# Kernel tuning notes

Hardware: AMD Instinct MI355X
Metric: run time of the kernel (lower is better)

The kernel has to match this reference:

```python
import jax, jax.numpy as jnp
import numpy as np

TOPK = 64  # init kwarg: number of dst routes kept per src node


def setup_inputs() -> dict:
    key = jax.random.key(0)
    ks = jax.random.split(key, 6)
    B, J, K, D, Dd = 4, 4096, 8192, 64, 64  # batch, src_nodes, dst_nodes, src_dim, dst_dim
    val = jax.random.normal(ks[0], (B, J, D), jnp.float32)
    state = jax.random.normal(ks[1], (B, J), jnp.float32)
    dst_state = jax.random.normal(ks[2], (B, K), jnp.float32)
    dst_val = jax.random.normal(ks[3], (B, K, Dd), jnp.float32)
    W_route = jax.random.normal(ks[4], (D, K), jnp.float32) / np.sqrt(D).astype(np.float32)
    W_val = jax.random.normal(ks[5], (D, Dd), jnp.float32) / np.sqrt(D).astype(np.float32)
    return dict(val=val, state=state, dst_state=dst_state, dst_val=dst_val,
                W_route=W_route, W_val=W_val)


def _sparse_routes(logits, topk):
    # top-k indices per src node, scatter a bool mask, masked softmax over dst axis
    _, idx = jax.lax.top_k(logits, topk)              # [B, J, topk]
    B, J, K = logits.shape
    mask = jnp.zeros((B, J, K), dtype=bool)
    mask = mask.at[jnp.arange(B)[:, None, None],
                   jnp.arange(J)[None, :, None], idx].set(True)
    neg = jnp.finfo(logits.dtype).min
    return jax.nn.softmax(jnp.where(mask, logits, neg), axis=-1)


def reference(val, state, dst_state, dst_val, W_route, W_val):
    # route_fn: linear over src val -> logits [B, J, K]
    logits = jnp.einsum('bjd,dk->bjk', val, W_route)
    routes = _sparse_routes(logits, TOPK)             # sparse masked softmax
    projected_val = jnp.einsum('bjd,de->bje', val, W_val)  # val_proj_fn (Linear)
    projected_state = state                            # state_proj_fn = Identity
    sender = jax.nn.softplus(state)                    # state_activation_fn
    weighted = routes * sender[..., None]              # [B, J, K]
    delta_state = jnp.einsum('bjk,bj->bk', weighted, projected_state)
    delta_val = jnp.einsum('bjk,bjd->bkd', weighted, projected_val)
    # merge_mode='add'
    return (dst_state + delta_state, dst_val + delta_val)
```

## Files before the change

kernel.cpp:

```cpp
#include <hip/hip_runtime.h>
#include <math.h>

#define NB 4
#define J 4096
#define KDIM 8192
#define DDIM 64
#define DD 64
#define TOPK 64

#define BM 32
#define THREADS 512
#define THREADS_SEL 256
#define NITER_H 8
#define CAP_H 128
#define GCAP 256
#define BCAP 96
#define OVFCAP 262144

typedef _Float16 half8_t __attribute__((ext_vector_type(8)));
typedef float f32x16 __attribute__((ext_vector_type(16)));
union H8 { half8_t h; uint4 u; };
__device__ __forceinline__ half8_t as_h8(uint4 v) { H8 x; x.u = v; return x.h; }

__device__ __forceinline__ unsigned f2key(float f) {
  unsigned u = __float_as_uint(f);
  return u ^ (unsigned)(((int)u >> 31) | 0x80000000);
}
__device__ __forceinline__ float key2f(unsigned k) {
  unsigned u = (k & 0x80000000u) ? (k & 0x7FFFFFFFu) : ~k;
  return __uint_as_float(u);
}
__device__ __forceinline__ unsigned wred_maxu(unsigned v) {
  #pragma unroll
  for (int o = 32; o > 0; o >>= 1) { unsigned u = __shfl_xor(v, o, 64); v = u > v ? u : v; }
  return v;
}
__device__ __forceinline__ unsigned wred_minu(unsigned v) {
  #pragma unroll
  for (int o = 32; o > 0; o >>= 1) { unsigned u = __shfl_xor(v, o, 64); v = u < v ? u : v; }
  return v;
}
__device__ __forceinline__ float wred_addf(float v) {
  #pragma unroll
  for (int o = 32; o > 0; o >>= 1) v += __shfl_xor(v, o, 64);
  return v;
}

__device__ __forceinline__ void route_append(
    unsigned* counts, uint2* bucket, unsigned* ovf_cnt, uint2* ovf,
    int b, unsigned kk, unsigned jloc, float w)
{
  const size_t bk = (size_t)b * KDIM + kk;
  const unsigned slot = atomicAdd(&counts[bk], 1u);
  if (slot < BCAP) {
    bucket[bk * BCAP + slot] = make_uint2(__float_as_uint(w), jloc);
  } else {
    const unsigned op = atomicAdd(ovf_cnt, 1u);
    if (op < (unsigned)OVFCAP)
      ovf[op] = make_uint2(__float_as_uint(w), ((unsigned)bk << 12) | jloc);
  }
}

__global__ void k_prep(const float* __restrict__ W, unsigned* __restrict__ WFh,
                       float* __restrict__ WT)
{
  __shared__ _Float16 lh[64][64];
  __shared__ float lf[64][64];
  const int t = threadIdx.x;
  const int kb = blockIdx.x * 64;
  for (int i = t; i < 4096; i += 256) {
    const int d = i >> 6, c = i & 63;
    const float x = W[(size_t)d * KDIM + kb + c];
    lh[c][d] = (_Float16)x;
    lf[c][d] = x;
  }
  __syncthreads();
  for (int q = t; q < 512; q += 256) {
    const int gt2 = q >> 8, rem = q & 255;
    const int ks = rem >> 6, lane = rem & 63;
    const int c = gt2 * 32 + (lane & 31);
    const int d0 = ks * 16 + (lane >> 5) * 8;
    const int gtile = blockIdx.x * 2 + gt2;
    const size_t off = ((size_t)(gtile * 4 + ks) * 64 + lane) * 4;
    *(uint4*)(WFh + off) = *(const uint4*)&lh[c][d0];
  }
  for (int q = t; q < 1024; q += 256) {
    const int c = q >> 4, d0 = (q & 15) * 4;
    *(float4*)(WT + (size_t)(kb + c) * DDIM + d0) = *(const float4*)&lf[c][d0];
  }
}

__global__ __launch_bounds__(THREADS, 4) void k_cand(
    const float* __restrict__ val, const unsigned* __restrict__ WFh,
    const float* __restrict__ W_val, float* __restrict__ pv,
    unsigned short* __restrict__ gidx, unsigned* __restrict__ gcnt,
    float* __restrict__ gtau, unsigned* __restrict__ flags)
{
  __shared__ __align__(16) float val_lds[BM][DDIM + 4];
  __shared__ unsigned short cand_idx[BM][CAP_H];
  __shared__ unsigned have[BM];
  __shared__ float tauF[BM];

  const int t = threadIdx.x;
  const int lane = t & 63;
  const int wv = t >> 6;
  const int hi = lane >> 5;
  const int lane31 = lane & 31;
  const int row0 = blockIdx.x * BM;
  const int h = blockIdx.y;

  {
    const int r = t >> 4, d0 = (t & 15) * 4;
    const float4 v4 = *(const float4*)(val + (size_t)(row0 + r) * DDIM + d0);
    val_lds[r][d0] = v4.x; val_lds[r][d0 + 1] = v4.y;
    val_lds[r][d0 + 2] = v4.z; val_lds[r][d0 + 3] = v4.w;
  }
  __syncthreads();

  if (t < BM) {
    float n2 = 0.f;
    #pragma unroll
    for (int d = 0; d < DDIM; ++d) { const float x = val_lds[t][d]; n2 = fmaf(x, x, n2); }
    tauF[t] = 0.26f * sqrtf(n2);
    have[t] = 0u;
    if (h == 0) gtau[row0 + t] = tauF[t];
  }

  half8_t ah[4];
  {
    const int m = lane31;
    #pragma unroll
    for (int ks = 0; ks < 4; ++ks) {
      const int d0 = ks * 16 + hi * 8;
      #pragma unroll
      for (int j = 0; j < 8; ++j) ah[ks][j] = (_Float16)val_lds[m][d0 + j];
    }
  }
  __syncthreads();

  float taufr[16];
  #pragma unroll
  for (int r = 0; r < 16; ++r) taufr[r] = tauF[(r & 3) + 8 * (r >> 2) + 4 * hi];

  const unsigned* wpBase = WFh + (size_t)(h * 128 + wv * 2) * 1024 + lane * 4;
  const unsigned* wp = wpBase;
  uint4 b0 = *(const uint4*)(wp);        uint4 b1 = *(const uint4*)(wp + 256);
  uint4 b2 = *(const uint4*)(wp + 512);  uint4 b3 = *(const uint4*)(wp + 768);
  uint4 b4 = *(const uint4*)(wp + 1024); uint4 b5 = *(const uint4*)(wp + 1280);
  uint4 b6 = *(const uint4*)(wp + 1536); uint4 b7 = *(const uint4*)(wp + 1792);

  #pragma unroll 1
  for (int it = 0; it < NITER_H; ++it) {
    f32x16 acc0, acc1;
    #pragma unroll
    for (int i = 0; i < 16; ++i) { acc0[i] = 0.f; acc1[i] = 0.f; }
    acc0 = __builtin_amdgcn_mfma_f32_32x32x16_f16(ah[0], as_h8(b0), acc0, 0, 0, 0);
    acc1 = __builtin_amdgcn_mfma_f32_32x32x16_f16(ah[0], as_h8(b4), acc1, 0, 0, 0);
    acc0 = __builtin_amdgcn_mfma_f32_32x32x16_f16(ah[1], as_h8(b1), acc0, 0, 0, 0);
    acc1 = __builtin_amdgcn_mfma_f32_32x32x16_f16(ah[1], as_h8(b5), acc1, 0, 0, 0);
    acc0 = __builtin_amdgcn_mfma_f32_32x32x16_f16(ah[2], as_h8(b2), acc0, 0, 0, 0);
    acc1 = __builtin_amdgcn_mfma_f32_32x32x16_f16(ah[2], as_h8(b6), acc1, 0, 0, 0);
    acc0 = __builtin_amdgcn_mfma_f32_32x32x16_f16(ah[3], as_h8(b3), acc0, 0, 0, 0);
    acc1 = __builtin_amdgcn_mfma_f32_32x32x16_f16(ah[3], as_h8(b7), acc1, 0, 0, 0);

    const unsigned colbase = (unsigned)((h * 128 + it * 16 + wv * 2) * 32 + lane31);

    wp = (it == NITER_H - 1) ? wpBase : wp + 16384;
    b0 = *(const uint4*)(wp);        b1 = *(const uint4*)(wp + 256);
    b2 = *(const uint4*)(wp + 512);  b3 = *(const uint4*)(wp + 768);
    b4 = *(const uint4*)(wp + 1024); b5 = *(const uint4*)(wp + 1280);
    b6 = *(const uint4*)(wp + 1536); b7 = *(const uint4*)(wp + 1792);

    #pragma unroll
    for (int r = 0; r < 16; ++r) {
      const int row = (r & 3) + 8 * (r >> 2) + 4 * hi;
      const float tf = taufr[r];
      if (acc0[r] > tf) {
        const unsigned slot = atomicAdd(&have[row], 1u);
        if (slot < CAP_H) cand_idx[row][slot] = (unsigned short)colbase;
      }
      if (acc1[r] > tf) {
        const unsigned slot = atomicAdd(&have[row], 1u);
        if (slot < CAP_H) cand_idx[row][slot] = (unsigned short)(colbase + 32);
      }
    }
  }

  if (h == 1) {
    const int r = t >> 4, e0 = (t & 15) * 4;
    float a0 = 0.f, a1 = 0.f, a2 = 0.f, a3 = 0.f;
    #pragma unroll 8
    for (int d = 0; d < DDIM; ++d) {
      const float v = val_lds[r][d];
      const float4 w4 = *(const float4*)(W_val + (size_t)d * DD + e0);
      a0 = fmaf(v, w4.x, a0); a1 = fmaf(v, w4.y, a1);
      a2 = fmaf(v, w4.z, a2); a3 = fmaf(v, w4.w, a3);
    }
    *(float4*)(pv + (size_t)(row0 + r) * DD + e0) = make_float4(a0, a1, a2, a3);
  }

  __syncthreads();

  for (int i = t; i < BM * CAP_H; i += THREADS) {
    const int r = i >> 7, s = i & (CAP_H - 1);
    const unsigned hv = have[r];
    const int lim = hv < CAP_H ? (int)hv : CAP_H;
    if (s < lim)
      gidx[(size_t)(row0 + r) * GCAP + h * CAP_H + s] = cand_idx[r][s];
  }
  if (t < BM) {
    const unsigned hv = have[t];
    gcnt[(size_t)(row0 + t) * 2 + h] = hv < CAP_H ? hv : CAP_H;
    if (hv > CAP_H) flags[row0 + t] = 1u;
  }
}

__global__ __launch_bounds__(THREADS_SEL, 4) void k_select(
    const float* __restrict__ val, const float* __restrict__ state,
    const float* __restrict__ WT,
    const unsigned short* __restrict__ gidx, const unsigned* __restrict__ gcnt,
    const float* __restrict__ gtau, unsigned* __restrict__ flags,
    unsigned* __restrict__ counts, uint2* __restrict__ bucket,
    unsigned* __restrict__ ovf_cnt, uint2* __restrict__ ovf)
{
  __shared__ float skey[THREADS_SEL / 64][GCAP];
  const int t = threadIdx.x;
  const int lane = t & 63;
  const int wv = t >> 6;
  const int row = blockIdx.x * (THREADS_SEL / 64) + wv;

  if (flags[row]) return;
  const int c0 = (int)gcnt[(size_t)row * 2];
  const int c1 = (int)gcnt[(size_t)row * 2 + 1];
  const int nc = c0 + c1;
  if (nc < TOPK) { if (lane == 0) flags[row] = 1u; return; }
  const float tau = gtau[row];

  const int cq = lane >> 2;
  const int dq = lane & 3;
  float4 v4[4];
  #pragma unroll
  for (int j = 0; j < 4; ++j)
    v4[j] = *(const float4*)(val + (size_t)row * DDIM + j * 16 + dq * 4);

  const unsigned short* grow = gidx + (size_t)row * GCAP;

  unsigned id4[4];
  #pragma unroll
  for (int i = 0; i < 4; ++i) {
    const int s = i * 64 + lane;
    id4[i] = 0xFFFFFFFFu;
    if (s < nc) {
      const int ps = s < c0 ? s : (s - c0 + CAP_H);
      id4[i] = (unsigned)grow[ps];
    }
  }

  for (int s0 = 0; s0 < nc; s0 += 32) {
    const int sA = s0 + cq;
    const int sB = s0 + 16 + cq;
    const bool okA = sA < nc, okB = sB < nc;
    int psA = sA < c0 ? sA : (sA - c0 + CAP_H); if (!okA) psA = 0;
    int psB = sB < c0 ? sB : (sB - c0 + CAP_H); if (!okB) psB = 0;
    const unsigned kkA = (unsigned)grow[psA] & (KDIM - 1);
    const unsigned kkB = (unsigned)grow[psB] & (KDIM - 1);
    const float* wtA = WT + (size_t)kkA * DDIM + dq * 4;
    const float* wtB = WT + (size_t)kkB * DDIM + dq * 4;
    float4 wA[4], wB[4];
    #pragma unroll
    for (int j = 0; j < 4; ++j) wA[j] = *(const float4*)(wtA + j * 16);
    #pragma unroll
    for (int j = 0; j < 4; ++j) wB[j] = *(const float4*)(wtB + j * 16);
    float aA = 0.f, aB = 0.f;
    #pragma unroll
    for (int j = 0; j < 4; ++j) {
      aA = fmaf(v4[j].x, wA[j].x, aA); aA = fmaf(v4[j].y, wA[j].y, aA);
      aA = fmaf(v4[j].z, wA[j].z, aA); aA = fmaf(v4[j].w, wA[j].w, aA);
      aB = fmaf(v4[j].x, wB[j].x, aB); aB = fmaf(v4[j].y, wB[j].y, aB);
      aB = fmaf(v4[j].z, wB[j].z, aB); aB = fmaf(v4[j].w, wB[j].w, aB);
    }
    aA += __shfl_xor(aA, 1, 64); aA += __shfl_xor(aA, 2, 64);
    aB += __shfl_xor(aB, 1, 64); aB += __shfl_xor(aB, 2, 64);
    if (dq == 0) {
      if (okA) skey[wv][sA] = aA;
      if (okB) skey[wv][sB] = aB;
    }
  }
  asm volatile("s_waitcnt lgkmcnt(0)" ::: "memory");
  __builtin_amdgcn_sched_barrier(0);

  unsigned k4[4];
  #pragma unroll
  for (int i = 0; i < 4; ++i) {
    const int s = i * 64 + lane;
    k4[i] = (s < nc) ? f2key(skey[wv][s]) : 0u;
  }
  unsigned lmax = k4[0];
  #pragma unroll
  for (int i = 1; i < 4; ++i) lmax = k4[i] > lmax ? k4[i] : lmax;
  const unsigned kmaxAll = wred_maxu(lmax);
  unsigned klo = f2key(0.99f * tau); if (klo == 0u) klo = 1u;
  unsigned khi = kmaxAll + 1u;
  auto cge4 = [&](unsigned th) {
    int c = 0;
    #pragma unroll
    for (int i = 0; i < 4; ++i) c += __popcll(__ballot(k4[i] >= th));
    return c;
  };
  int cnt = nc;
  while (cnt != TOPK && khi - klo > 1u) {
    const unsigned mid = klo + ((khi - klo) >> 1);
    const int c = cge4(mid);
    if (c >= TOPK) { klo = mid; cnt = c; } else khi = mid;
  }
  const unsigned thr = klo;
  if (key2f(thr) <= 1.006f * tau) {
    if (lane == 0) flags[row] = 1u;
    return;
  }
  unsigned selmask = 0u;
  if (cnt == TOPK) {
    #pragma unroll
    for (int i = 0; i < 4; ++i) if (k4[i] >= thr) selmask |= 1u << i;
  } else {
    #pragma unroll
    for (int i = 0; i < 4; ++i) if (k4[i] > thr) selmask |= 1u << i;
    int tot = 0;
    #pragma unroll
    for (int i = 0; i < 4; ++i) tot += __popcll(__ballot((selmask >> i) & 1));
    int need = TOPK - tot;
    while (need > 0) {
      unsigned best = 0xFFFFFFFFu; int bi = -1;
      #pragma unroll
      for (int i = 0; i < 4; ++i)
        if (k4[i] == thr && !(selmask & (1u << i)) && id4[i] < best) { best = id4[i]; bi = i; }
      const unsigned g = wred_minu(best);
      if (g == 0xFFFFFFFFu) break;
      if (bi >= 0 && best == g) selmask |= 1u << bi;
      --need;
    }
  }
  const float m = key2f(kmaxAll);
  float p[4]; float lsum = 0.f;
  #pragma unroll
  for (int i = 0; i < 4; ++i) {
    p[i] = 0.f;
    if (selmask & (1u << i)) { p[i] = __expf(key2f(k4[i]) - m); lsum += p[i]; }
  }
  lsum = wred_addf(lsum);
  const float st = state[row];
  const float sender = st > 20.f ? st : log1pf(__expf(st));
  const float scale = sender / lsum;
  const int b = row / J;
  const unsigned jloc = (unsigned)(row & (J - 1));
  #pragma unroll
  for (int i = 0; i < 4; ++i) {
    if (selmask & (1u << i))
      route_append(counts, bucket, ovf_cnt, ovf, b, id4[i], jloc, p[i] * scale);
  }
}

__global__ void k_fix(const float* __restrict__ val, const float* __restrict__ state,
                      const float* __restrict__ W, const unsigned* __restrict__ flags,
                      unsigned* __restrict__ counts, uint2* __restrict__ bucket,
                      unsigned* __restrict__ ovf_cnt, uint2* __restrict__ ovf)
{
  __shared__ unsigned anyf;
  __shared__ unsigned lsk[64][TOPK + 1];
  __shared__ unsigned short lsi[64][TOPK];
  const int t = threadIdx.x;
  const int row = blockIdx.x * 64 + t;
  if (t == 0) anyf = 0u;
  __syncthreads();
  const unsigned f = flags[row];
  if (f) anyf = 1u;
  __syncthreads();
  if (!anyf) return;
  if (!f) return;

  float v[DDIM];
  #pragma unroll
  for (int d = 0; d < DDIM; ++d) v[d] = val[(size_t)row * DDIM + d];
  int m = 0, worst = 0;
  for (int k = 0; k < KDIM; ++k) {
    float acc = 0.f;
    #pragma unroll 8
    for (int d = 0; d < DDIM; ++d) acc = fmaf(v[d], W[(size_t)d * KDIM + k], acc);
    const unsigned key = f2key(acc);
    if (m < TOPK) {
      lsk[t][m] = key; lsi[t][m] = (unsigned short)k; ++m;
      if (m == TOPK) {
        worst = 0;
        for (int q = 1; q < TOPK; ++q)
          if (lsk[t][q] < lsk[t][worst] ||
              (lsk[t][q] == lsk[t][worst] && lsi[t][q] > lsi[t][worst])) worst = q;
      }
    } else if (key > lsk[t][worst]) {
      lsk[t][worst] = key; lsi[t][worst] = (unsigned short)k;
      worst = 0;
      for (int q = 1; q < TOPK; ++q)
        if (lsk[t][q] < lsk[t][worst] ||
            (lsk[t][q] == lsk[t][worst] && lsi[t][q] > lsi[t][worst])) worst = q;
    }
  }
  unsigned km = lsk[t][0];
  for (int q = 1; q < TOPK; ++q) if (lsk[t][q] > km) km = lsk[t][q];
  const float mx = key2f(km);
  float lsum = 0.f;
  for (int q = 0; q < TOPK; ++q) lsum += __expf(key2f(lsk[t][q]) - mx);
  const float st = state[row];
  const float sender = st > 20.f ? st : log1pf(__expf(st));
  const float scale = sender / lsum;
  const int b = row / J;
  const unsigned jloc = (unsigned)(row & (J - 1));
  for (int q = 0; q < TOPK; ++q) {
    const float w = __expf(key2f(lsk[t][q]) - mx) * scale;
    route_append(counts, bucket, ovf_cnt, ovf, b, (unsigned)lsi[t][q], jloc, w);
  }
}

__global__ void k_gather(const unsigned* __restrict__ counts,
                         const uint2* __restrict__ bucket, const float* __restrict__ pv,
                         const float* __restrict__ state,
                         const float* __restrict__ dst_state,
                         const float* __restrict__ dst_val,
                         float* __restrict__ out_state, float* __restrict__ out_val)
{
  const int wv = threadIdx.x >> 6, lane = threadIdx.x & 63;
  const size_t bk = (size_t)blockIdx.x * 4 + wv;
  unsigned n = counts[bk];
  if (n > BCAP) n = BCAP;
  const int b = (int)(bk >> 13);
  const size_t jbase = (size_t)b * J;
  const uint2* __restrict__ bb = bucket + bk * BCAP;
  float a0 = 0.f, a1 = 0.f, a2 = 0.f, a3 = 0.f;
  float s0 = 0.f, s1 = 0.f, s2 = 0.f, s3 = 0.f;
  unsigned i = 0;
  for (; i + 4 <= n; i += 4) {
    const uint2 e0 = bb[i + 0], e1 = bb[i + 1], e2 = bb[i + 2], e3 = bb[i + 3];
    const float w0 = __uint_as_float(e0.x), w1 = __uint_as_float(e1.x);
    const float w2 = __uint_as_float(e2.x), w3 = __uint_as_float(e3.x);
    a0 = fmaf(w0, pv[(jbase + e0.y) * DD + lane], a0);
    a1 = fmaf(w1, pv[(jbase + e1.y) * DD + lane], a1);
    a2 = fmaf(w2, pv[(jbase + e2.y) * DD + lane], a2);
    a3 = fmaf(w3, pv[(jbase + e3.y) * DD + lane], a3);
    s0 = fmaf(w0, state[jbase + e0.y], s0); s1 = fmaf(w1, state[jbase + e1.y], s1);
    s2 = fmaf(w2, state[jbase + e2.y], s2); s3 = fmaf(w3, state[jbase + e3.y], s3);
  }
  for (; i < n; ++i) {
    const uint2 e = bb[i];
    const float w = __uint_as_float(e.x);
    a0 = fmaf(w, pv[(jbase + e.y) * DD + lane], a0);
    s0 = fmaf(w, state[jbase + e.y], s0);
  }
  const size_t o = bk * DD + lane;
  out_val[o] = dst_val[o] + ((a0 + a1) + (a2 + a3));
  if (lane == 0) out_state[bk] = dst_state[bk] + ((s0 + s1) + (s2 + s3));
}

__global__ void k_ovf(const unsigned* __restrict__ ovf_cnt, const uint2* __restrict__ ovf,
                      const float* __restrict__ pv, const float* __restrict__ state,
                      float* __restrict__ out_state, float* __restrict__ out_val)
{
  unsigned n = *ovf_cnt;
  if (n > (unsigned)OVFCAP) n = (unsigned)OVFCAP;
  const unsigned wglob = (blockIdx.x * blockDim.x + threadIdx.x) >> 6;
  const int lane = threadIdx.x & 63;
  const unsigned nw = (gridDim.x * blockDim.x) >> 6;
  for (unsigned i = wglob; i < n; i += nw) {
    const uint2 e = ovf[i];
    const float w = __uint_as_float(e.x);
    const unsigned bk = e.y >> 12;
    const unsigned j = e.y & (J - 1);
    const size_t jg = (size_t)(bk >> 13) * J + j;
    atomicAdd(&out_val[(size_t)bk * DD + lane], w * pv[jg * DD + lane]);
    if (lane == 0) atomicAdd(&out_state[bk], w * state[jg]);
  }
}

extern "C" void kernel_launch(void* const* d_in, const int* in_sizes, int n_in,
                              void* d_out, int out_size, void* d_ws, size_t ws_size,
                              hipStream_t stream)
{
  (void)in_sizes; (void)n_in; (void)out_size; (void)ws_size;
  const float* val       = (const float*)d_in[0];
  const float* state     = (const float*)d_in[1];
  const float* dst_state = (const float*)d_in[2];
  const float* dst_val   = (const float*)d_in[3];
  const float* W_route   = (const float*)d_in[4];
  const float* W_val     = (const float*)d_in[5];
  float* out_state = (float*)d_out;
  float* out_val   = out_state + (size_t)NB * KDIM;

  char* p = (char*)d_ws;
  unsigned* counts  = (unsigned*)p;  p += (size_t)NB * KDIM * 4;
  unsigned* flags   = (unsigned*)p;  p += (size_t)NB * J * 4;
  unsigned* ovf_cnt = (unsigned*)p;  p += 256;
  unsigned* gcnt    = (unsigned*)p;  p += (size_t)NB * J * 2 * 4;
  float* pv         = (float*)p;     p += (size_t)NB * J * DD * 4;
  unsigned* WFh     = (unsigned*)p;  p += (size_t)KDIM * DDIM * 2;
  float* WT         = (float*)p;     p += (size_t)KDIM * DDIM * 4;
  float* gtau       = (float*)p;     p += (size_t)NB * J * 4;
  unsigned short* gidx = (unsigned short*)p; p += (size_t)NB * J * GCAP * 2;
  uint2* bucket     = (uint2*)p;     p += (size_t)NB * KDIM * BCAP * 8;
  uint2* ovf        = (uint2*)p;     p += (size_t)OVFCAP * 8;

  hipMemsetAsync(counts, 0,
                 (size_t)NB * KDIM * 4 + (size_t)NB * J * 4 + 256 +
                 (size_t)NB * J * 2 * 4, stream);

  hipLaunchKernelGGL(k_prep, dim3(KDIM / 64), dim3(256), 0, stream, W_route, WFh, WT);
  hipLaunchKernelGGL(k_cand, dim3(NB * J / BM, 2), dim3(THREADS), 0, stream,
                     val, WFh, W_val, pv, gidx, gcnt, gtau, flags);
  hipLaunchKernelGGL(k_select, dim3(NB * J / (THREADS_SEL / 64)), dim3(THREADS_SEL),
                     0, stream, val, state, WT, gidx, gcnt, gtau, flags,
                     counts, bucket, ovf_cnt, ovf);
  hipLaunchKernelGGL(k_fix, dim3(NB * J / 64), dim3(64), 0, stream,
                     val, state, W_route, flags, counts, bucket, ovf_cnt, ovf);
  hipLaunchKernelGGL(k_gather, dim3(NB * KDIM / 4), dim3(256), 0, stream,
                     counts, bucket, pv, state, dst_state, dst_val, out_state, out_val);
  hipLaunchKernelGGL(k_ovf, dim3(256), dim3(256), 0, stream,
                     ovf_cnt, ovf, pv, state, out_state, out_val);
}
```

Measured before the change: 197.5 us.

## Shard route buckets by dst group and XCD, accumulate gather in LDS

Route entries are now appended to per-(batch, 32-dst group, XCD) shard lists rather than per-destination buckets. This spreads atomic counter contention across XCDs and groups writes for neighbouring destinations together. The gather kernel now runs one block per dst group, broadcasts entries with shuffles and accumulates into per-wave LDS tiles before writing outputs. This lowers the count of tiny per-destination lists, at the cost of LDS read-modify-write traffic, divergent accumulation and a different overflow distribution.

Result: slower. 324.6 us (+64.4%).

```diff
diff --git a/kernel.cpp b/kernel.cpp
--- a/kernel.cpp
+++ b/kernel.cpp
@@ -14,8 +14,13 @@
 #define NITER_H 8
 #define CAP_H 128
 #define GCAP 256
-#define BCAP 96
 #define OVFCAP 262144
+
+#define KG 32
+#define NKG (KDIM / KG)
+#define NSHARD (NB * NKG * 8)
+#define SHCAP 384
+#define GW 4
 
 typedef _Float16 half8_t __attribute__((ext_vector_type(8)));
 typedef float f32x16 __attribute__((ext_vector_type(16)));
@@ -47,17 +52,20 @@
 }
 
 __device__ __forceinline__ void route_append(
-    unsigned* counts, uint2* bucket, unsigned* ovf_cnt, uint2* ovf,
-    int b, unsigned kk, unsigned jloc, float w)
-{
-  const size_t bk = (size_t)b * KDIM + kk;
-  const unsigned slot = atomicAdd(&counts[bk], 1u);
-  if (slot < BCAP) {
-    bucket[bk * BCAP + slot] = make_uint2(__float_as_uint(w), jloc);
+    unsigned* shcnt, uint2* shlist, unsigned* ovf_cnt, uint2* ovf,
+    int b, int xcd, unsigned kk, unsigned jloc, float w)
+{
+  const unsigned g = (unsigned)b * NKG + (kk >> 5);
+  const unsigned shard = (g << 3) | (unsigned)xcd;
+  const unsigned slot = atomicAdd(&shcnt[shard], 1u);
+  if (slot < SHCAP) {
+    shlist[(size_t)shard * SHCAP + slot] =
+        make_uint2(__float_as_uint(w), ((kk & (KG - 1)) << 12) | jloc);
   } else {
     const unsigned op = atomicAdd(ovf_cnt, 1u);
     if (op < (unsigned)OVFCAP)
-      ovf[op] = make_uint2(__float_as_uint(w), ((unsigned)bk << 12) | jloc);
+      ovf[op] = make_uint2(__float_as_uint(w),
+                           (((unsigned)b * KDIM + kk) << 12) | jloc);
   }
 }
 
@@ -220,7 +228,7 @@
     const float* __restrict__ WT,
     const unsigned short* __restrict__ gidx, const unsigned* __restrict__ gcnt,
     const float* __restrict__ gtau, unsigned* __restrict__ flags,
-    unsigned* __restrict__ counts, uint2* __restrict__ bucket,
+    unsigned* __restrict__ shcnt, uint2* __restrict__ shlist,
     unsigned* __restrict__ ovf_cnt, uint2* __restrict__ ovf)
 {
   __shared__ float skey[THREADS_SEL / 64][GCAP];
@@ -228,6 +236,7 @@
   const int lane = t & 63;
   const int wv = t >> 6;
   const int row = blockIdx.x * (THREADS_SEL / 64) + wv;
+  const int xcd = blockIdx.x & 7;
 
   if (flags[row]) return;
   const int c0 = (int)gcnt[(size_t)row * 2];
@@ -356,13 +365,13 @@
   #pragma unroll
   for (int i = 0; i < 4; ++i) {
     if (selmask & (1u << i))
-      route_append(counts, bucket, ovf_cnt, ovf, b, id4[i], jloc, p[i] * scale);
+      route_append(shcnt, shlist, ovf_cnt, ovf, b, xcd, id4[i], jloc, p[i] * scale);
   }
 }
 
 __global__ void k_fix(const float* __restrict__ val, const float* __restrict__ state,
                       const float* __restrict__ W, const unsigned* __restrict__ flags,
-                      unsigned* __restrict__ counts, uint2* __restrict__ bucket,
+                      unsigned* __restrict__ shcnt, uint2* __restrict__ shlist,
                       unsigned* __restrict__ ovf_cnt, uint2* __restrict__ ovf)
 {
   __shared__ unsigned anyf;
@@ -370,6 +379,7 @@
   __shared__ unsigned short lsi[64][TOPK];
   const int t = threadIdx.x;
   const int row = blockIdx.x * 64 + t;
+  const int xcd = blockIdx.x & 7;
   if (t == 0) anyf = 0u;
   __syncthreads();
   const unsigned f = flags[row];
@@ -415,47 +425,77 @@
   const unsigned jloc = (unsigned)(row & (J - 1));
   for (int q = 0; q < TOPK; ++q) {
     const float w = __expf(key2f(lsk[t][q]) - mx) * scale;
-    route_append(counts, bucket, ovf_cnt, ovf, b, (unsigned)lsi[t][q], jloc, w);
-  }
-}
-
-__global__ void k_gather(const unsigned* __restrict__ counts,
-                         const uint2* __restrict__ bucket, const float* __restrict__ pv,
-                         const float* __restrict__ state,
-                         const float* __restrict__ dst_state,
-                         const float* __restrict__ dst_val,
-                         float* __restrict__ out_state, float* __restrict__ out_val)
-{
-  const int wv = threadIdx.x >> 6, lane = threadIdx.x & 63;
-  const size_t bk = (size_t)blockIdx.x * 4 + wv;
-  unsigned n = counts[bk];
-  if (n > BCAP) n = BCAP;
-  const int b = (int)(bk >> 13);
+    route_append(shcnt, shlist, ovf_cnt, ovf, b, xcd, (unsigned)lsi[t][q], jloc, w);
+  }
+}
+
+__global__ __launch_bounds__(256, 4) void k_gather(
+    const unsigned* __restrict__ shcnt, const uint2* __restrict__ shlist,
+    const float* __restrict__ pv, const float* __restrict__ state,
+    const float* __restrict__ dst_state, const float* __restrict__ dst_val,
+    float* __restrict__ out_state, float* __restrict__ out_val)
+{
+  __shared__ float accv[GW][KG][DD + 1];
+  const int t = threadIdx.x;
+  const int lane = t & 63;
+  const int wv = t >> 6;
+  const int b  = blockIdx.x >> 8;
+  const int kg = blockIdx.x & (NKG - 1);
   const size_t jbase = (size_t)b * J;
-  const uint2* __restrict__ bb = bucket + bk * BCAP;
-  float a0 = 0.f, a1 = 0.f, a2 = 0.f, a3 = 0.f;
-  float s0 = 0.f, s1 = 0.f, s2 = 0.f, s3 = 0.f;
-  unsigned i = 0;
-  for (; i + 4 <= n; i += 4) {
-    const uint2 e0 = bb[i + 0], e1 = bb[i + 1], e2 = bb[i + 2], e3 = bb[i + 3];
-    const float w0 = __uint_as_float(e0.x), w1 = __uint_as_float(e1.x);
-    const float w2 = __uint_as_float(e2.x), w3 = __uint_as_float(e3.x);
-    a0 = fmaf(w0, pv[(jbase + e0.y) * DD + lane], a0);
-    a1 = fmaf(w1, pv[(jbase + e1.y) * DD + lane], a1);
-    a2 = fmaf(w2, pv[(jbase + e2.y) * DD + lane], a2);
-    a3 = fmaf(w3, pv[(jbase + e3.y) * DD + lane], a3);
-    s0 = fmaf(w0, state[jbase + e0.y], s0); s1 = fmaf(w1, state[jbase + e1.y], s1);
-    s2 = fmaf(w2, state[jbase + e2.y], s2); s3 = fmaf(w3, state[jbase + e3.y], s3);
-  }
-  for (; i < n; ++i) {
-    const uint2 e = bb[i];
-    const float w = __uint_as_float(e.x);
-    a0 = fmaf(w, pv[(jbase + e.y) * DD + lane], a0);
-    s0 = fmaf(w, state[jbase + e.y], s0);
-  }
-  const size_t o = bk * DD + lane;
-  out_val[o] = dst_val[o] + ((a0 + a1) + (a2 + a3));
-  if (lane == 0) out_state[bk] = dst_state[bk] + ((s0 + s1) + (s2 + s3));
+
+  for (int i = t; i < GW * KG * (DD + 1); i += 256) ((float*)accv)[i] = 0.f;
+  __syncthreads();
+
+  const int gbase = (b * NKG + kg) << 3;
+  for (int x = 0; x < 8; ++x) {
+    const unsigned n0 = shcnt[gbase + x];
+    const unsigned n = n0 < SHCAP ? n0 : SHCAP;
+    const uint2* lst = shlist + (size_t)(gbase + x) * SHCAP;
+    for (unsigned base = (unsigned)wv * 64; base < n; base += GW * 64) {
+      const uint2 e = lst[base + lane];
+      const int mrem = (int)(n - base);
+      const int mm = mrem < 64 ? mrem : 64;
+      const float sOwn = (lane < mm) ? state[jbase + (e.y & (J - 1))] : 0.f;
+      for (int c0 = 0; c0 < mm; c0 += 8) {
+        float pw[8], vv[8], sv[8]; int kk[8], ok[8];
+        #pragma unroll
+        for (int i = 0; i < 8; ++i) {
+          const int c = (c0 + i) & 63;
+          const unsigned ex = __shfl(e.x, c, 64);
+          const unsigned ey = __shfl(e.y, c, 64);
+          ok[i] = (c0 + i) < mm;
+          pw[i] = __uint_as_float(ex);
+          kk[i] = (int)((ey >> 12) & (KG - 1));
+          const unsigned j = ey & (J - 1);
+          vv[i] = ok[i] ? pv[(jbase + j) * DD + lane] : 0.f;
+          sv[i] = __shfl(sOwn, c, 64);
+        }
+        #pragma unroll
+        for (int i = 0; i < 8; ++i) {
+          if (ok[i]) {
+            accv[wv][kk[i]][lane] += pw[i] * vv[i];
+            if (lane == 0) accv[wv][kk[i]][DD] += pw[i] * sv[i];
+          }
+        }
+      }
+    }
+  }
+  __syncthreads();
+
+  const int k0 = kg * KG;
+  for (int i = t; i < KG * DD; i += 256) {
+    const int k = i >> 6, d = i & 63;
+    const float s = ((accv[0][k][d] + accv[1][k][d]) +
+                     (accv[2][k][d] + accv[3][k][d]));
+    const size_t o = ((size_t)b * KDIM + k0 + k) * DD + d;
+    out_val[o] = dst_val[o] + s;
+  }
+  if (t < KG) {
+    const float s = ((accv[0][t][DD] + accv[1][t][DD]) +
+                     (accv[2][t][DD] + accv[3][t][DD]));
+    const size_t o = (size_t)b * KDIM + k0 + t;
+    out_state[o] = dst_state[o] + s;
+  }
 }
 
 __global__ void k_ovf(const unsigned* __restrict__ ovf_cnt, const uint2* __restrict__ ovf,
@@ -493,7 +533,7 @@
   float* out_val   = out_state + (size_t)NB * KDIM;
 
   char* p = (char*)d_ws;
-  unsigned* counts  = (unsigned*)p;  p += (size_t)NB * KDIM * 4;
+  unsigned* shcnt   = (unsigned*)p;  p += (size_t)NSHARD * 4;
   unsigned* flags   = (unsigned*)p;  p += (size_t)NB * J * 4;
   unsigned* ovf_cnt = (unsigned*)p;  p += 256;
   unsigned* gcnt    = (unsigned*)p;  p += (size_t)NB * J * 2 * 4;
@@ -502,11 +542,11 @@
   float* WT         = (float*)p;     p += (size_t)KDIM * DDIM * 4;
   float* gtau       = (float*)p;     p += (size_t)NB * J * 4;
   unsigned short* gidx = (unsigned short*)p; p += (size_t)NB * J * GCAP * 2;
-  uint2* bucket     = (uint2*)p;     p += (size_t)NB * KDIM * BCAP * 8;
+  uint2* shlist     = (uint2*)p;     p += (size_t)NSHARD * SHCAP * 8;
   uint2* ovf        = (uint2*)p;     p += (size_t)OVFCAP * 8;
 
-  hipMemsetAsync(counts, 0,
-                 (size_t)NB * KDIM * 4 + (size_t)NB * J * 4 + 256 +
+  hipMemsetAsync(shcnt, 0,
+                 (size_t)NSHARD * 4 + (size_t)NB * J * 4 + 256 +
                  (size_t)NB * J * 2 * 4, stream);
 
   hipLaunchKernelGGL(k_prep, dim3(KDIM / 64), dim3(256), 0, stream, W_route, WFh, WT);
@@ -514,11 +554,11 @@
                      val, WFh, W_val, pv, gidx, gcnt, gtau, flags);
   hipLaunchKernelGGL(k_select, dim3(NB * J / (THREADS_SEL / 64)), dim3(THREADS_SEL),
                      0, stream, val, state, WT, gidx, gcnt, gtau, flags,
-                     counts, bucket, ovf_cnt, ovf);
+                     shcnt, shlist, ovf_cnt, ovf);
   hipLaunchKernelGGL(k_fix, dim3(NB * J / 64), dim3(64), 0, stream,
-                     val, state, W_route, flags, counts, bucket, ovf_cnt, ovf);
-  hipLaunchKernelGGL(k_gather, dim3(NB * KDIM / 4), dim3(256), 0, stream,
-                     counts, bucket, pv, state, dst_state, dst_val, out_state, out_val);
+                     val, state, W_route, flags, shcnt, shlist, ovf_cnt, ovf);
+  hipLaunchKernelGGL(k_gather, dim3(NB * NKG), dim3(256), 0, stream,
+                     shcnt, shlist, pv, state, dst_state, dst_val, out_state, out_val);
   hipLaunchKernelGGL(k_ovf, dim3(256), dim3(256), 0, stream,
                      ovf_cnt, ovf, pv, state, out_state, out_val);
 }
```
